# Kernel optimization log

Measured on AMD Instinct MI355X. Metric: run time of the kernel, lower is better.

## Reference

```python
import jax, jax.numpy as jnp
import numpy as np

NA = 3        # num anchors
NM = 32       # num prototype masks
NC = 80       # num classes
STRIDE = 8    # network stride
THRESH = 0.05 # conf threshold


def setup_inputs() -> dict:
    key = jax.random.key(0)
    nB, nH, nW = 16, 80, 80
    channels = NA * (5 + NC) + NA * NM  # 351
    output = jax.random.normal(key, (nB, channels, nH, nW), dtype=jnp.float32)
    # anchors already in output-grid units (pixel anchors / stride), shape [NA, 2] = (w, h)
    anchors = jnp.array([[1.25, 1.625], [2.0, 3.75], [4.125, 2.875]], dtype=jnp.float32)
    return {"output": output, "anchors": anchors}


def reference(output, anchors):
    nB, channels, nH, nW = output.shape
    nHW = nH * nW
    # split box head and mask-coefficient head
    box = output[:, :NA * (5 + NC)].reshape(nB, NA, 5 + NC, nHW)
    mask_out = output[:, NA * (5 + NC):].reshape(nB, NA, NM, nHW).transpose(0, 1, 3, 2)  # [nB,NA,nHW,NM]

    lin_y, lin_x = jnp.meshgrid(jnp.arange(nH, dtype=output.dtype),
                                jnp.arange(nW, dtype=output.dtype), indexing='ij')
    lin_x = lin_x.reshape(-1)
    lin_y = lin_y.reshape(-1)

    anchor_wh = anchors.reshape(1, NA, 2, 1)  # broadcast over [nB,NA,2,nHW]
    max_value = jnp.floor(jnp.log(jnp.asarray(1e35, output.dtype) / anchors.max() / STRIDE))

    xs = jax.nn.sigmoid(box[:, :, 0]) + lin_x                                   # [nB,NA,nHW]
    ys = jax.nn.sigmoid(box[:, :, 1]) + lin_y                                   # [nB,NA,nHW]
    wh = jnp.exp(jnp.minimum(box[:, :, 2:4], max_value)) * anchor_wh            # [nB,NA,2,nHW]
    obj = jax.nn.sigmoid(box[:, :, 4])                                          # [nB,NA,nHW]

    cls = jax.nn.softmax(box[:, :, 5:], axis=2)                                 # [nB,NA,NC,nHW]
    cls_max = cls.max(axis=2)
    cls_idx = cls.argmax(axis=2).astype(output.dtype)
    score = cls_max * obj                                                        # [nB,NA,nHW]

    keep = score > THRESH
    b, a, p = jnp.nonzero(keep)  # eager: data-dependent detection count N

    coords = jnp.stack([xs[b, a, p], ys[b, a, p], wh[b, a, 0, p], wh[b, a, 1, p]], axis=1) * STRIDE  # [N,4]
    mc = mask_out[b, a, p]                                                        # [N,NM]
    return jnp.concatenate([
        b[:, None].astype(output.dtype),
        coords,
        mc,
        score[b, a, p][:, None],
        cls_idx[b, a, p][:, None],
    ], axis=1)  # [N, 7+NM]
```

## Files before the change

### kernel.cpp

```cpp
#include <hip/hip_runtime.h>
#include <math.h>

#define NA 3
#define NM 32
#define NC 80
#define STRIDE_PX 8.0f
#define THRESH 0.05f
#define NB 16
#define NH 80
#define NW 80
#define NHW (NH * NW)
#define CH (NA * (5 + NC) + NA * NM)
#define BOXCH (NA * (5 + NC))
#define TOTAL (NB * NA * NHW)
#define BLK 256
#define NBLK (TOTAL / BLK)
#define ROWSZ (7 + NM)
#define WS_ROW_STRIDE (BLK * ROWSZ)

__device__ __forceinline__ int wave_sum64(int v) {
#pragma unroll
  for (int s = 32; s > 0; s >>= 1) v += __shfl_xor(v, s, 64);
  return v;
}

__global__ __launch_bounds__(BLK) void decode_kernel(
    const float* __restrict__ in, const float* __restrict__ anchors,
    float* __restrict__ wsrows, int* __restrict__ counts) {
  int g = blockIdx.x * BLK + threadIdx.x;
  int p = g % NHW;
  int a = (g / NHW) % NA;
  int b = g / (NA * NHW);

  const float* base = in + ((size_t)b * CH + (size_t)a * (5 + NC)) * NHW + p;

  float tx = base[0];
  float ty = base[(size_t)1 * NHW];
  float tw = base[(size_t)2 * NHW];
  float th = base[(size_t)3 * NHW];
  float tobj = base[(size_t)4 * NHW];

  float m = -INFINITY, s = 0.f;
  int idx = 0;
#pragma unroll
  for (int j = 0; j < NC; ++j) {
    float x = base[(size_t)(5 + j) * NHW];
    float mn = fmaxf(m, x);
    s = s * __expf(m - mn) + __expf(x - mn);
    idx = (x > m) ? j : idx;
    m = mn;
  }

  float cls_max = 1.0f / s;
  float obj = 1.0f / (1.0f + __expf(-tobj));
  float score = cls_max * obj;

  float amax = fmaxf(fmaxf(fmaxf(anchors[0], anchors[1]), fmaxf(anchors[2], anchors[3])),
                     fmaxf(anchors[4], anchors[5]));
  float max_value = floorf(logf(1e35f / amax / STRIDE_PX));
  float aw = anchors[a * 2 + 0];
  float ah = anchors[a * 2 + 1];

  float xs = 1.0f / (1.0f + __expf(-tx)) + (float)(p % NW);
  float ys = 1.0f / (1.0f + __expf(-ty)) + (float)(p / NW);
  float w = __expf(fminf(tw, max_value)) * aw;
  float h = __expf(fminf(th, max_value)) * ah;

  bool keep = score > THRESH;
  unsigned long long ball = __ballot(keep);
  int lane = threadIdx.x & 63;
  int wv = threadIdx.x >> 6;
  int lower = __popcll(ball & ((1ull << lane) - 1ull));
  __shared__ int wc[BLK / 64];
  if (lane == 0) wc[wv] = __popcll(ball);
  __syncthreads();
  int pre = 0;
#pragma unroll
  for (int i = 0; i < BLK / 64; ++i)
    if (i < wv) pre += wc[i];

  if (keep) {
    int lrank = pre + lower;
    float* o = wsrows + (size_t)blockIdx.x * WS_ROW_STRIDE + (size_t)lrank * ROWSZ;
    o[0] = (float)b;
    o[1] = xs * STRIDE_PX;
    o[2] = ys * STRIDE_PX;
    o[3] = w * STRIDE_PX;
    o[4] = h * STRIDE_PX;
    const float* mbase = in + ((size_t)b * CH + BOXCH + (size_t)a * NM) * NHW + p;
#pragma unroll
    for (int mm = 0; mm < NM; ++mm) o[5 + mm] = mbase[(size_t)mm * NHW];
    o[5 + NM] = score;
    o[6 + NM] = (float)idx;
  }
  if (threadIdx.x == 0)
    counts[blockIdx.x] = wc[0] + wc[1] + wc[2] + wc[3];
}

__global__ __launch_bounds__(BLK) void emit_kernel(
    const float* __restrict__ wsrows, const int* __restrict__ counts,
    float* __restrict__ out, int out_size) {
  int bid = blockIdx.x;
  int t = threadIdx.x;

  int partial = 0;
  for (int j = t; j < bid; j += BLK) partial += counts[j];
  partial = wave_sum64(partial);
  __shared__ int sh[BLK / 64];
  if ((t & 63) == 0) sh[t >> 6] = partial;
  __syncthreads();
  int off = sh[0] + sh[1] + sh[2] + sh[3];

  int cnt = counts[bid];
  int nelem = cnt * ROWSZ;
  const float* src = wsrows + (size_t)bid * WS_ROW_STRIDE;
  int dbase = off * ROWSZ;
  for (int e = t; e < nelem; e += BLK) {
    int d = dbase + e;
    if (d < out_size) out[d] = src[e];
  }
}

extern "C" void kernel_launch(void* const* d_in, const int* in_sizes, int n_in,
                              void* d_out, int out_size, void* d_ws, size_t ws_size,
                              hipStream_t stream) {
  const float* in = (const float*)d_in[0];
  const float* anchors = (const float*)d_in[1];

  float* wsrows = (float*)d_ws;
  int* counts = (int*)((float*)d_ws + (size_t)NBLK * WS_ROW_STRIDE);

  decode_kernel<<<NBLK, BLK, 0, stream>>>(in, anchors, wsrows, counts);
  emit_kernel<<<NBLK, BLK, 0, stream>>>(wsrows, counts, (float*)d_out, out_size);
}
```

Measured before the change: 226.5 us.

## Chunk softmax reduction, pad workspace rows for float4 stores, add occupancy hints

The serial online-softmax over 80 classes becomes 16-wide chunks with tree max/argmax and tree sums, which shortens the dependency chain and lets loads issue in batches. Workspace rows are padded from 39 to 40 floats so decode can write each detection with float4 stores, and emit remaps indices with a magic-number divide to compact the rows. Launch bounds gain minimum-occupancy hints. The chunked loads need more registers, and the tie-breaking for argmax must still pick the first maximum.

Result: no change. 226.4 us (median of 2 runs) (-0.0%).

```diff
diff --git a/kernel.cpp b/kernel.cpp
--- a/kernel.cpp
+++ b/kernel.cpp
@@ -15,8 +15,9 @@
 #define TOTAL (NB * NA * NHW)
 #define BLK 256
 #define NBLK (TOTAL / BLK)
-#define ROWSZ (7 + NM)
-#define WS_ROW_STRIDE (BLK * ROWSZ)
+#define ROWSZ 39
+#define ROWPAD 40
+#define WS_ROW_STRIDE (BLK * ROWPAD)
 
 __device__ __forceinline__ int wave_sum64(int v) {
 #pragma unroll
@@ -24,7 +25,7 @@
   return v;
 }
 
-__global__ __launch_bounds__(BLK) void decode_kernel(
+__global__ __launch_bounds__(BLK, 6) void decode_kernel(
     const float* __restrict__ in, const float* __restrict__ anchors,
     float* __restrict__ wsrows, int* __restrict__ counts) {
   int g = blockIdx.x * BLK + threadIdx.x;
@@ -43,11 +44,50 @@
   float m = -INFINITY, s = 0.f;
   int idx = 0;
 #pragma unroll
-  for (int j = 0; j < NC; ++j) {
-    float x = base[(size_t)(5 + j) * NHW];
-    float mn = fmaxf(m, x);
-    s = s * __expf(m - mn) + __expf(x - mn);
-    idx = (x > m) ? j : idx;
+  for (int c = 0; c < NC; c += 16) {
+    float x[16];
+#pragma unroll
+    for (int j = 0; j < 16; ++j) x[j] = base[(size_t)(5 + c + j) * NHW];
+
+    float m8[8]; int i8[8];
+#pragma unroll
+    for (int k = 0; k < 8; ++k) {
+      bool gt = x[2 * k + 1] > x[2 * k];
+      m8[k] = gt ? x[2 * k + 1] : x[2 * k];
+      i8[k] = gt ? (2 * k + 1) : (2 * k);
+    }
+    float m4[4]; int i4[4];
+#pragma unroll
+    for (int k = 0; k < 4; ++k) {
+      bool gt = m8[2 * k + 1] > m8[2 * k];
+      m4[k] = gt ? m8[2 * k + 1] : m8[2 * k];
+      i4[k] = gt ? i8[2 * k + 1] : i8[2 * k];
+    }
+    float m2[2]; int i2[2];
+#pragma unroll
+    for (int k = 0; k < 2; ++k) {
+      bool gt = m4[2 * k + 1] > m4[2 * k];
+      m2[k] = gt ? m4[2 * k + 1] : m4[2 * k];
+      i2[k] = gt ? i4[2 * k + 1] : i4[2 * k];
+    }
+    bool gtc = m2[1] > m2[0];
+    float mc = gtc ? m2[1] : m2[0];
+    int ic = (gtc ? i2[1] : i2[0]) + c;
+
+    float e[16];
+#pragma unroll
+    for (int j = 0; j < 16; ++j) e[j] = __expf(x[j] - mc);
+    float s8[8];
+#pragma unroll
+    for (int k = 0; k < 8; ++k) s8[k] = e[2 * k] + e[2 * k + 1];
+    float s4[4];
+#pragma unroll
+    for (int k = 0; k < 4; ++k) s4[k] = s8[2 * k] + s8[2 * k + 1];
+    float sc = (s4[0] + s4[1]) + (s4[2] + s4[3]);
+
+    float mn = fmaxf(m, mc);
+    s = s * __expf(m - mn) + sc * __expf(mc - mn);
+    idx = (mc > m) ? ic : idx;
     m = mn;
   }
 
@@ -81,23 +121,31 @@
 
   if (keep) {
     int lrank = pre + lower;
-    float* o = wsrows + (size_t)blockIdx.x * WS_ROW_STRIDE + (size_t)lrank * ROWSZ;
-    o[0] = (float)b;
-    o[1] = xs * STRIDE_PX;
-    o[2] = ys * STRIDE_PX;
-    o[3] = w * STRIDE_PX;
-    o[4] = h * STRIDE_PX;
+    float4* o4 = reinterpret_cast<float4*>(
+        wsrows + (size_t)blockIdx.x * WS_ROW_STRIDE + (size_t)lrank * ROWPAD);
     const float* mbase = in + ((size_t)b * CH + BOXCH + (size_t)a * NM) * NHW + p;
+
+    float4 v;
+    v.x = (float)b; v.y = xs * STRIDE_PX; v.z = ys * STRIDE_PX; v.w = w * STRIDE_PX;
+    o4[0] = v;
+    v.x = h * STRIDE_PX; v.y = mbase[0]; v.z = mbase[(size_t)1 * NHW]; v.w = mbase[(size_t)2 * NHW];
+    o4[1] = v;
 #pragma unroll
-    for (int mm = 0; mm < NM; ++mm) o[5 + mm] = mbase[(size_t)mm * NHW];
-    o[5 + NM] = score;
-    o[6 + NM] = (float)idx;
+    for (int gq = 2; gq <= 8; ++gq) {
+      v.x = mbase[(size_t)(4 * gq - 5) * NHW];
+      v.y = mbase[(size_t)(4 * gq - 4) * NHW];
+      v.z = mbase[(size_t)(4 * gq - 3) * NHW];
+      v.w = mbase[(size_t)(4 * gq - 2) * NHW];
+      o4[gq] = v;
+    }
+    v.x = mbase[(size_t)31 * NHW]; v.y = score; v.z = (float)idx; v.w = 0.f;
+    o4[9] = v;
   }
   if (threadIdx.x == 0)
     counts[blockIdx.x] = wc[0] + wc[1] + wc[2] + wc[3];
 }
 
-__global__ __launch_bounds__(BLK) void emit_kernel(
+__global__ __launch_bounds__(BLK, 8) void emit_kernel(
     const float* __restrict__ wsrows, const int* __restrict__ counts,
     float* __restrict__ out, int out_size) {
   int bid = blockIdx.x;
@@ -116,8 +164,10 @@
   const float* src = wsrows + (size_t)bid * WS_ROW_STRIDE;
   int dbase = off * ROWSZ;
   for (int e = t; e < nelem; e += BLK) {
+    int row = (int)(((unsigned)e * 107547u) >> 22);
+    int col = e - row * 39;
     int d = dbase + e;
-    if (d < out_size) out[d] = src[e];
+    if (d < out_size) out[d] = src[row * ROWPAD + col];
   }
 }
 
```
